# Kernel tuning notes

Hardware: AMD Instinct MI355X
Metric: run time of the kernel (lower is better)

The kernel has to match this reference:

```python
import jax, jax.numpy as jnp
import numpy as np

N, L, D = 1024, 128, 512
H = D // 2  # LSTM hidden per direction


def _lstm_dir(x, w_ih, w_hh, b_ih, b_hh, reverse=False):
    # x: [B, T, Din] -> [B, T, H]; PyTorch gate order i, f, g, o
    B = x.shape[0]
    Hh = w_hh.shape[1]
    xs = jnp.swapaxes(x, 0, 1)  # [T, B, Din]
    if reverse:
        xs = xs[::-1]
    pre = jnp.einsum('tbi,gi->tbg', xs, w_ih) + b_ih  # precompute input contribution

    def step(carry, p):
        h, c = carry
        g = p + h @ w_hh.T + b_hh
        i, f, cc, o = jnp.split(g, 4, axis=-1)
        c = jax.nn.sigmoid(f) * c + jax.nn.sigmoid(i) * jnp.tanh(cc)
        h = jax.nn.sigmoid(o) * jnp.tanh(c)
        return (h, c), h

    zeros = jnp.zeros((B, Hh), x.dtype)
    _, hs = jax.lax.scan(step, (zeros, zeros), pre)
    if reverse:
        hs = hs[::-1]
    return jnp.swapaxes(hs, 0, 1)


def _bilstm(x, params):
    # params: [(w_ih, w_hh, b_ih, b_hh)] for l0_fwd, l0_bwd, l1_fwd, l1_bwd
    for lf, lb in ((params[0], params[1]), (params[2], params[3])):
        f = _lstm_dir(x, *lf)
        b = _lstm_dir(x, *lb, reverse=True)
        x = jnp.concatenate([f, b], axis=-1)
    return x


def _forward(episodes, query, current_state, ages, Wq, bq, Wk, bk, lstm_params, k):
    # retrieve_relevant_episodes: batched version of the per-episode loop
    query_proj = query @ Wq.T + bq              # [D]
    emb = episodes.mean(axis=1)                 # [N, D] per-episode mean embedding
    key_proj = emb @ Wk.T + bk                  # [N, D]
    scores = key_proj @ query_proj              # [N] (matmul(q, kp.T).mean() == dot for 1D)
    _, idx = jax.lax.top_k(scores, k)           # descending, == argsort[-k:][::-1]
    sel = jnp.take(episodes, idx, axis=0)       # [k, L, D]
    # temporal_attention
    w = 1.0 / (1.0 + jnp.take(ages, idx) * 0.01)  # temporal recency weight
    x = sel * w[:, None, None]
    lstm_out = _bilstm(x, lstm_params)          # [k, L, D]
    att = jnp.einsum('d,kld->kl', current_state, lstm_out)  # [k, L] (== [k,1,L])
    attw = jax.nn.softmax(att, axis=-1)
    context = jnp.einsum('kl,kld->kd', attw, lstm_out)[:, None, :]  # [k, 1, D]
    return context


def setup_inputs() -> dict:
    key = jax.random.key(0)
    ks = jax.random.split(key, 32)
    s = 1.0 / np.sqrt(D)
    sh = 1.0 / np.sqrt(H)
    inp = {
        'episodes': jax.random.normal(ks[0], (N, L, D), jnp.float32),
        'query': jax.random.normal(ks[1], (D,), jnp.float32),
        'current_state': jax.random.normal(ks[2], (D,), jnp.float32),
        'ages': jax.random.uniform(ks[3], (N,), jnp.float32) * 100.0,
        'Wq': jax.random.normal(ks[4], (D, D), jnp.float32) * s,
        'bq': jnp.zeros((D,), jnp.float32),
        'Wk': jax.random.normal(ks[5], (D, D), jnp.float32) * s,
        'bk': jnp.zeros((D,), jnp.float32),
    }
    i = 6
    for name in ['l0', 'l0r', 'l1', 'l1r']:
        inp['w_ih_' + name] = jax.random.normal(ks[i], (4 * H, D), jnp.float32) * sh; i += 1
        inp['w_hh_' + name] = jax.random.normal(ks[i], (4 * H, H), jnp.float32) * sh; i += 1
        inp['b_ih_' + name] = jnp.zeros((4 * H,), jnp.float32)
        inp['b_hh_' + name] = jnp.zeros((4 * H,), jnp.float32)
    inp['k'] = 5
    return inp


def reference(episodes, query, current_state, ages, Wq, bq, Wk, bk,
              w_ih_l0, w_hh_l0, b_ih_l0, b_hh_l0,
              w_ih_l0r, w_hh_l0r, b_ih_l0r, b_hh_l0r,
              w_ih_l1, w_hh_l1, b_ih_l1, b_hh_l1,
              w_ih_l1r, w_hh_l1r, b_ih_l1r, b_hh_l1r, k):
    lstm_params = [
        (w_ih_l0, w_hh_l0, b_ih_l0, b_hh_l0),
        (w_ih_l0r, w_hh_l0r, b_ih_l0r, b_hh_l0r),
        (w_ih_l1, w_hh_l1, b_ih_l1, b_hh_l1),
        (w_ih_l1r, w_hh_l1r, b_ih_l1r, b_hh_l1r),
    ]
    return _forward(episodes, query, current_state, ages, Wq, bq, Wk, bk, lstm_params, k)
```

## Files before the change

### kernel.cpp

```cpp
#include <hip/hip_runtime.h>
#include <hip/hip_bf16.h>
#include <math.h>

typedef unsigned short u16;
typedef unsigned int   u32;
typedef unsigned long long u64;

#define DEV static __device__ __forceinline__

static constexpr int LL = 128, DD = 512, HH = 256, KK = 5, NN = 1024;

static constexpr size_t OFF_QP   = 0;
static constexpr size_t OFF_U    = 4096;
static constexpr size_t OFF_CC   = 8192;
static constexpr size_t OFF_SC   = 12288;
static constexpr size_t OFF_WSC  = 16384;
static constexpr size_t OFF_IDX  = 16640;
static constexpr size_t OFF_HG   = 20480;
static constexpr size_t OFF_PRE  = 102400;
static constexpr size_t OFF_OUT0 = OFF_PRE  + (size_t)2*LL*5*1024*4;
static constexpr size_t OFF_OUT1 = OFF_OUT0 + (size_t)5*LL*DD*4;

DEV float sigf(float x){ return 1.0f/(1.0f + expf(-x)); }

__global__ void k_qproj(const float* __restrict__ Wq, const float* __restrict__ q,
                        const float* __restrict__ bq, float* __restrict__ qp) {
  __shared__ float qs[512];
  int tid = threadIdx.x;
  qs[tid] = q[tid]; qs[tid+256] = q[tid+256];
  __syncthreads();
  int row  = blockIdx.x*8 + (tid >> 5);
  int lane = tid & 31;
  const float* wr = Wq + (size_t)row*512 + lane*16;
  float acc = 0.f;
  #pragma unroll
  for (int j = 0; j < 16; j += 4) {
    float4 w = *(const float4*)(wr + j);
    acc += w.x*qs[lane*16+j] + w.y*qs[lane*16+j+1] + w.z*qs[lane*16+j+2] + w.w*qs[lane*16+j+3];
  }
  #pragma unroll
  for (int off = 16; off > 0; off >>= 1) acc += __shfl_down(acc, off, 32);
  if (lane == 0) qp[row] = acc + bq[row];
}

__global__ void k_keyvec(const float* __restrict__ Wk, const float* __restrict__ bk,
                         const float* __restrict__ qp, float* __restrict__ u,
                         float* __restrict__ cconst) {
  __shared__ float qs[512];
  __shared__ float red[16][17];
  __shared__ float r2[256];
  int tid = threadIdx.x;
  qs[tid] = qp[tid]; qs[tid+256] = qp[tid+256];
  __syncthreads();
  int cl = tid & 15;
  int jc = tid >> 4;
  int col = blockIdx.x*16 + cl;
  float acc = 0.f;
  for (int j = jc*32; j < jc*32 + 32; ++j) acc += Wk[(size_t)j*512 + col] * qs[j];
  red[cl][jc] = acc;
  __syncthreads();
  if (tid < 16) {
    float a = 0.f;
    #pragma unroll
    for (int m = 0; m < 16; ++m) a += red[tid][m];
    u[blockIdx.x*16 + tid] = a;
  }
  if (blockIdx.x == 0) {
    float b2 = bk[tid]*qs[tid] + bk[tid+256]*qs[tid+256];
    r2[tid] = b2;
    __syncthreads();
    for (int off = 128; off > 0; off >>= 1) { if (tid < off) r2[tid] += r2[tid+off]; __syncthreads(); }
    if (tid == 0) cconst[0] = r2[0];
  }
}

__global__ void k_scores(const float* __restrict__ ep, const float* __restrict__ u,
                         const float* __restrict__ cconst, float* __restrict__ scores) {
  __shared__ float red[256];
  int tid = threadIdx.x, n = blockIdx.x;
  int d0 = (tid * 4) & 511;
  float u0 = u[d0+0], u1 = u[d0+1], u2 = u[d0+2], u3 = u[d0+3];
  const float* base = ep + (size_t)n * (LL*DD);
  float acc = 0.f;
  for (int c = tid; c < (LL*DD)/4; c += 256) {
    float4 v = *(const float4*)(base + (size_t)c*4);
    acc += v.x*u0 + v.y*u1 + v.z*u2 + v.w*u3;
  }
  red[tid] = acc;
  __syncthreads();
  for (int off = 128; off > 0; off >>= 1) { if (tid < off) red[tid] += red[tid+off]; __syncthreads(); }
  if (tid == 0) scores[n] = red[0] * (1.0f/LL) + cconst[0];
}

__global__ void k_topk(const float* __restrict__ scores, const float* __restrict__ ages,
                       int* __restrict__ idx5, float* __restrict__ wsc) {
  __shared__ float s0[NN];
  __shared__ float sv[NN];
  __shared__ int   si[NN];
  __shared__ int   chosen[KK];
  int tid = threadIdx.x;
  s0[tid] = scores[tid];
  __syncthreads();
  for (int r = 0; r < KK; ++r) {
    float v = s0[tid];
    for (int m = 0; m < r; ++m) if (chosen[m] == tid) v = -3.4e38f;
    sv[tid] = v; si[tid] = tid;
    __syncthreads();
    for (int off = 512; off > 0; off >>= 1) {
      if (tid < off) {
        float a = sv[tid], b = sv[tid+off];
        int ia = si[tid], ib = si[tid+off];
        if (b > a || (b == a && ib < ia)) { sv[tid] = b; si[tid] = ib; }
      }
      __syncthreads();
    }
    if (tid == 0) {
      int w = si[0];
      chosen[r] = w;
      idx5[r] = w;
      wsc[r] = 1.0f / (1.0f + ages[w] * 0.01f);
    }
    __syncthreads();
  }
}

__global__ void k_pre(const float* __restrict__ ep, const float* __restrict__ x1,
                      const int* __restrict__ idx5, const float* __restrict__ wsc,
                      const float* __restrict__ wihF, const float* __restrict__ wihB,
                      const float* __restrict__ bihF, const float* __restrict__ bhhF,
                      const float* __restrict__ bihB, const float* __restrict__ bhhB,
                      float* __restrict__ pre) {
  int t = blockIdx.x, rb = blockIdx.y, dir = blockIdx.z;
  int tid = threadIdx.x;
  __shared__ __align__(16) float xs[5*512];
  __shared__ __align__(16) float wt[256*36];
  if (ep) {
    for (int f = tid; f < 5*512; f += 256) {
      int b = f >> 9, i = f & 511;
      xs[f] = ep[((size_t)idx5[b]*LL + t)*DD + i] * wsc[b];
    }
  } else {
    for (int f = tid; f < 5*512; f += 256) {
      int b = f >> 9, i = f & 511;
      xs[f] = x1[((size_t)b*LL + t)*DD + i];
    }
  }
  const float* wih = dir ? wihB : wihF;
  const float* bih = dir ? bihB : bihF;
  const float* bhh = dir ? bhhB : bhhF;
  int r0 = rb * 256;
  float acc[5] = {0,0,0,0,0};
  for (int it = 0; it < 16; ++it) {
    __syncthreads();
    for (int c = tid; c < 2048; c += 256) {
      int rr = c >> 3;
      int ii = (c & 7) * 4;
      *(float4*)&wt[rr*36 + ii] = *(const float4*)&wih[(size_t)(r0+rr)*512 + it*32 + ii];
    }
    __syncthreads();
    const float* wrow = &wt[(size_t)tid*36];
    const float* xb = &xs[it*32];
    for (int ii = 0; ii < 32; ii += 4) {
      float4 w = *(const float4*)(wrow + ii);
      #pragma unroll
      for (int b = 0; b < 5; ++b) {
        float4 xv = *(const float4*)&xb[b*512 + ii];
        acc[b] += w.x*xv.x + w.y*xv.y + w.z*xv.z + w.w*xv.w;
      }
    }
  }
  int grow = r0 + tid;
  float bias = bih[grow] + bhh[grow];
  size_t pbase = (((size_t)dir*LL + t)*5)*1024 + grow;
  #pragma unroll
  for (int b = 0; b < 5; ++b) pre[pbase + (size_t)b*1024] = acc[b] + bias;
}

__global__ __launch_bounds__(1024) void k_lstm(
    const float* __restrict__ whhF, const float* __restrict__ whhB,
    const float* __restrict__ pre, float* __restrict__ out,
    u64* __restrict__ hg) {
  int wg  = blockIdx.x;
  int dir = wg >> 3;
  int q   = wg & 7;
  int tid = threadIdx.x;
  int p   = tid & 127;
  int jq  = tid >> 7;
  int jb  = jq * 32;
  const float* whh = dir ? whhB : whhF;

  __shared__ __align__(16) float h_lds[5*256];
  __shared__ float part[128*5*9];
  __shared__ float c_s[5*32];
  __shared__ float pre_lds[2*5*128];

  int gr = (p >> 5) * 256 + q * 32 + (p & 31);
  float w[32];
  #pragma unroll
  for (int m4 = 0; m4 < 8; ++m4) {
    float4 a = *(const float4*)(whh + (size_t)gr*256 + jb + m4*4);
    w[m4*4+0] = a.x; w[m4*4+1] = a.y; w[m4*4+2] = a.z; w[m4*4+3] = a.w;
  }
  for (int f = tid; f < 1280; f += 1024) h_lds[f] = 0.f;
  if (tid < 160) c_s[tid] = 0.f;
  u64* hg_dir = hg + (size_t)dir * 2 * 1280;

  if (tid < 640) {
    int t0 = dir ? (LL-1) : 0;
    int b = tid >> 7, r = tid & 127;
    int grow = (r >> 5)*256 + q*32 + (r & 31);
    pre_lds[tid] = pre[(((size_t)dir*LL + t0)*5 + b)*1024 + grow];
  }
  __syncthreads();

  for (int s = 0; s < LL; ++s) {
    int par = s & 1;
    int t = dir ? (LL-1-s) : s;
    float acc[5];
    #pragma unroll
    for (int b = 0; b < 5; ++b) {
      const float4* h4 = (const float4*)&h_lds[b*256 + jb];
      float a = 0.f;
      #pragma unroll
      for (int m4 = 0; m4 < 8; ++m4) {
        float4 hv = h4[m4];
        a += w[m4*4+0]*hv.x + w[m4*4+1]*hv.y + w[m4*4+2]*hv.z + w[m4*4+3]*hv.w;
      }
      acc[b] = a;
    }
    #pragma unroll
    for (int b = 0; b < 5; ++b) part[(p*5 + b)*9 + jq] = acc[b];
    __syncthreads();
    if (tid < 160) {
      int b = tid >> 5, u = tid & 31;
      float g[4];
      #pragma unroll
      for (int gate = 0; gate < 4; ++gate) {
        int r = gate*32 + u;
        float sum = pre_lds[par*640 + b*128 + r];
        #pragma unroll
        for (int m = 0; m < 8; ++m) sum += part[(r*5 + b)*9 + m];
        g[gate] = sum;
      }
      float ig = sigf(g[0]), fg = sigf(g[1]), cc = tanhf(g[2]), og = sigf(g[3]);
      float cn = fg * c_s[b*32 + u] + ig * cc;
      float hv = og * tanhf(cn);
      u64* hwr = hg_dir + (size_t)((s + 1) & 1) * 1280;
      u64 pk = ((u64)(u32)(s + 1) << 32) | (u64)__float_as_uint(hv);
      __hip_atomic_store(&hwr[b*256 + q*32 + u], pk,
                         __ATOMIC_RELAXED, __HIP_MEMORY_SCOPE_AGENT);
      c_s[b*32 + u] = cn;
      out[((size_t)b*LL + t)*DD + dir*HH + q*32 + u] = hv;
      h_lds[b*256 + q*32 + u] = hv;
    }
    float pfv = 0.f; int pfok = 0;
    if (tid >= 256 && tid < 896 && s + 1 < LL) {
      int f = tid - 256;
      int b = f >> 7, r = f & 127;
      int tn = dir ? (LL-2-s) : (s+1);
      int grow = (r >> 5)*256 + q*32 + (r & 31);
      pfv = pre[(((size_t)dir*LL + tn)*5 + b)*1024 + grow];
      pfok = 1;
    }
    if (tid >= 160 && s + 1 < LL) {
      int sp = s + 1;
      const u64* hrd = hg_dir + (size_t)(sp & 1) * 1280;
      int f0 = tid - 160;
      int f1 = f0 + 864;
      bool has2 = (f1 < 1280);
      u64 v0 = __hip_atomic_load(&hrd[f0], __ATOMIC_RELAXED, __HIP_MEMORY_SCOPE_AGENT);
      u64 v1 = has2 ? __hip_atomic_load(&hrd[f1], __ATOMIC_RELAXED, __HIP_MEMORY_SCOPE_AGENT)
                    : 0ull;
      bool d0 = false, d1 = !has2;
      while (!(d0 && d1)) {
        if (!d0) {
          if ((u32)(v0 >> 32) == (u32)sp) { h_lds[f0] = __uint_as_float((u32)v0); d0 = true; }
          else v0 = __hip_atomic_load(&hrd[f0], __ATOMIC_RELAXED, __HIP_MEMORY_SCOPE_AGENT);
        }
        if (!d1) {
          if ((u32)(v1 >> 32) == (u32)sp) { h_lds[f1] = __uint_as_float((u32)v1); d1 = true; }
          else v1 = __hip_atomic_load(&hrd[f1], __ATOMIC_RELAXED, __HIP_MEMORY_SCOPE_AGENT);
        }
      }
    }
    if (pfok) pre_lds[((par^1))*640 + (tid - 256)] = pfv;
    __syncthreads();
  }
}

__global__ void k_attn(const float* __restrict__ out1, const float* __restrict__ csb,
                       float* __restrict__ outp) {
  int b = blockIdx.x, tid = threadIdx.x;
  __shared__ float cs[512];
  __shared__ float att[128];
  __shared__ float red[256];
  __shared__ float smax, ssum;
  cs[tid] = csb[tid]; cs[tid+256] = csb[tid+256];
  __syncthreads();
  {
    int t = tid & 127, half = tid >> 7;
    const float* row = out1 + ((size_t)b*LL + t)*DD + half*256;
    const float* c2 = cs + half*256;
    float a = 0.f;
    for (int d = 0; d < 256; ++d) a += row[d] * c2[d];
    red[tid] = a;
  }
  __syncthreads();
  if (tid < 128) att[tid] = red[tid] + red[tid+128];
  __syncthreads();
  if (tid < 64) red[tid] = fmaxf(att[tid], att[tid+64]);
  __syncthreads();
  if (tid == 0) { float m = red[0]; for (int o = 1; o < 64; ++o) m = fmaxf(m, red[o]); smax = m; }
  __syncthreads();
  if (tid < 128) att[tid] = expf(att[tid] - smax);
  __syncthreads();
  if (tid < 64) red[tid] = att[tid] + att[tid+64];
  __syncthreads();
  if (tid == 0) { float s = 0.f; for (int o = 0; o < 64; ++o) s += red[o]; ssum = s; }
  __syncthreads();
  float inv = 1.0f / ssum;
  for (int d = tid; d < DD; d += 256) {
    float acc = 0.f;
    for (int t2 = 0; t2 < LL; ++t2) acc += att[t2] * out1[((size_t)b*LL + t2)*DD + d];
    outp[b*DD + d] = acc * inv;
  }
}

extern "C" void kernel_launch(void* const* d_in, const int* in_sizes, int n_in,
                              void* d_out, int out_size, void* d_ws, size_t ws_size,
                              hipStream_t stream) {
  (void)in_sizes; (void)n_in; (void)out_size; (void)ws_size;
  const float* ep   = (const float*)d_in[0];
  const float* qu   = (const float*)d_in[1];
  const float* cst  = (const float*)d_in[2];
  const float* ages = (const float*)d_in[3];
  const float* Wq   = (const float*)d_in[4];
  const float* bq   = (const float*)d_in[5];
  const float* Wk   = (const float*)d_in[6];
  const float* bk   = (const float*)d_in[7];
  const float *wih[4], *whh[4], *bih[4], *bhh[4];
  for (int l = 0; l < 4; ++l) {
    wih[l] = (const float*)d_in[8 + l*4 + 0];
    whh[l] = (const float*)d_in[8 + l*4 + 1];
    bih[l] = (const float*)d_in[8 + l*4 + 2];
    bhh[l] = (const float*)d_in[8 + l*4 + 3];
  }
  char* ws = (char*)d_ws;
  float* qp   = (float*)(ws + OFF_QP);
  float* uvec = (float*)(ws + OFF_U);
  float* cc   = (float*)(ws + OFF_CC);
  float* sc   = (float*)(ws + OFF_SC);
  float* wsc  = (float*)(ws + OFF_WSC);
  int*   idx5 = (int*)  (ws + OFF_IDX);
  u64*   hg0  = (u64*)  (ws + OFF_HG);
  u64*   hg1  = (u64*)  (ws + OFF_HG + 40960);
  float* pre  = (float*)(ws + OFF_PRE);
  float* out0 = (float*)(ws + OFF_OUT0);
  float* out1 = (float*)(ws + OFF_OUT1);

  hipMemsetAsync(ws + OFF_HG, 0, 81920, stream);

  k_qproj <<<64, 256, 0, stream>>>(Wq, qu, bq, qp);
  k_keyvec<<<32, 256, 0, stream>>>(Wk, bk, qp, uvec, cc);
  k_scores<<<NN, 256, 0, stream>>>(ep, uvec, cc, sc);
  k_topk  <<<1, 1024, 0, stream>>>(sc, ages, idx5, wsc);

  k_pre <<<dim3(LL,4,2), 256, 0, stream>>>(ep, nullptr, idx5, wsc,
        wih[0], wih[1], bih[0], bhh[0], bih[1], bhh[1], pre);
  k_lstm<<<16, 1024, 0, stream>>>(whh[0], whh[1], pre, out0, hg0);

  k_pre <<<dim3(LL,4,2), 256, 0, stream>>>(nullptr, out0, idx5, wsc,
        wih[2], wih[3], bih[2], bhh[2], bih[3], bhh[3], pre);
  k_lstm<<<16, 1024, 0, stream>>>(whh[2], whh[3], pre, out1, hg1);

  k_attn<<<KK, 256, 0, stream>>>(out1, cst, (float*)d_out);
}
```

Measured before the change: 1.525 ms.

## Interleave forward and backward LSTM directions in one workgroup to hide exchange latency

Each workgroup now handles one hidden slice for both directions, holding both recurrent weight slices in registers and alternating forward and backward steps. While one direction's gate math runs, the other threads poll the global h exchange for the opposite direction, so cross-workgroup sync latency overlaps with compute. A lighter barrier macro replaces __syncthreads. The grid is halved to 8 workgroups, which doubles register pressure per thread and puts both directions' serial work on the same workgroups.

```diff
diff --git a/kernel.cpp b/kernel.cpp
--- a/kernel.cpp
+++ b/kernel.cpp
@@ -22,6 +22,12 @@
 static constexpr size_t OFF_OUT1 = OFF_OUT0 + (size_t)5*LL*DD*4;
 
 DEV float sigf(float x){ return 1.0f/(1.0f + expf(-x)); }
+
+#define WGBAR() do { \
+  asm volatile("s_waitcnt lgkmcnt(0)" ::: "memory"); \
+  __builtin_amdgcn_s_barrier(); \
+  __builtin_amdgcn_sched_barrier(0); \
+} while (0)
 
 __global__ void k_qproj(const float* __restrict__ Wq, const float* __restrict__ q,
                         const float* __restrict__ bq, float* __restrict__ qp) {
@@ -180,111 +186,186 @@
     const float* __restrict__ whhF, const float* __restrict__ whhB,
     const float* __restrict__ pre, float* __restrict__ out,
     u64* __restrict__ hg) {
-  int wg  = blockIdx.x;
-  int dir = wg >> 3;
-  int q   = wg & 7;
+  int q   = blockIdx.x;
   int tid = threadIdx.x;
   int p   = tid & 127;
   int jq  = tid >> 7;
   int jb  = jq * 32;
-  const float* whh = dir ? whhB : whhF;
-
-  __shared__ __align__(16) float h_lds[5*256];
+
+  __shared__ __align__(16) float hF[5*256];
+  __shared__ __align__(16) float hB[5*256];
   __shared__ float part[128*5*9];
-  __shared__ float c_s[5*32];
-  __shared__ float pre_lds[2*5*128];
+  __shared__ float csF[160], csB[160];
+  __shared__ float preF[2*640], preB[2*640];
 
   int gr = (p >> 5) * 256 + q * 32 + (p & 31);
-  float w[32];
+  float wf[32], wb[32];
   #pragma unroll
   for (int m4 = 0; m4 < 8; ++m4) {
-    float4 a = *(const float4*)(whh + (size_t)gr*256 + jb + m4*4);
-    w[m4*4+0] = a.x; w[m4*4+1] = a.y; w[m4*4+2] = a.z; w[m4*4+3] = a.w;
-  }
-  for (int f = tid; f < 1280; f += 1024) h_lds[f] = 0.f;
-  if (tid < 160) c_s[tid] = 0.f;
-  u64* hg_dir = hg + (size_t)dir * 2 * 1280;
+    float4 a = *(const float4*)(whhF + (size_t)gr*256 + jb + m4*4);
+    wf[m4*4+0] = a.x; wf[m4*4+1] = a.y; wf[m4*4+2] = a.z; wf[m4*4+3] = a.w;
+    float4 c = *(const float4*)(whhB + (size_t)gr*256 + jb + m4*4);
+    wb[m4*4+0] = c.x; wb[m4*4+1] = c.y; wb[m4*4+2] = c.z; wb[m4*4+3] = c.w;
+  }
+  for (int f = tid; f < 1280; f += 1024) { hF[f] = 0.f; hB[f] = 0.f; }
+  if (tid < 160) { csF[tid] = 0.f; csB[tid] = 0.f; }
+  u64* hgF = hg;
+  u64* hgB = hg + 2560;
 
   if (tid < 640) {
-    int t0 = dir ? (LL-1) : 0;
     int b = tid >> 7, r = tid & 127;
     int grow = (r >> 5)*256 + q*32 + (r & 31);
-    pre_lds[tid] = pre[(((size_t)dir*LL + t0)*5 + b)*1024 + grow];
+    preF[tid] = pre[((size_t)(0*LL + 0)*5 + b)*1024 + grow];
+    preB[tid] = pre[((size_t)(1*LL + (LL-1))*5 + b)*1024 + grow];
   }
   __syncthreads();
 
   for (int s = 0; s < LL; ++s) {
-    int par = s & 1;
-    int t = dir ? (LL-1-s) : s;
-    float acc[5];
-    #pragma unroll
-    for (int b = 0; b < 5; ++b) {
-      const float4* h4 = (const float4*)&h_lds[b*256 + jb];
-      float a = 0.f;
-      #pragma unroll
-      for (int m4 = 0; m4 < 8; ++m4) {
-        float4 hv = h4[m4];
-        a += w[m4*4+0]*hv.x + w[m4*4+1]*hv.y + w[m4*4+2]*hv.z + w[m4*4+3]*hv.w;
-      }
-      acc[b] = a;
-    }
-    #pragma unroll
-    for (int b = 0; b < 5; ++b) part[(p*5 + b)*9 + jq] = acc[b];
-    __syncthreads();
+    int par  = s & 1;
+    int parn = (s + 1) & 1;
+    int tF = s, tB = LL - 1 - s;
+
+    {
+      float acc[5];
+      #pragma unroll
+      for (int b = 0; b < 5; ++b) {
+        const float4* h4 = (const float4*)&hF[b*256 + jb];
+        float a = 0.f;
+        #pragma unroll
+        for (int m4 = 0; m4 < 8; ++m4) {
+          float4 hv = h4[m4];
+          a += wf[m4*4+0]*hv.x + wf[m4*4+1]*hv.y + wf[m4*4+2]*hv.z + wf[m4*4+3]*hv.w;
+        }
+        acc[b] = a;
+      }
+      #pragma unroll
+      for (int b = 0; b < 5; ++b) part[(p*5 + b)*9 + jq] = acc[b];
+    }
+    WGBAR();
+
     if (tid < 160) {
       int b = tid >> 5, u = tid & 31;
       float g[4];
       #pragma unroll
       for (int gate = 0; gate < 4; ++gate) {
         int r = gate*32 + u;
-        float sum = pre_lds[par*640 + b*128 + r];
+        float sum = preF[par*640 + b*128 + r];
         #pragma unroll
         for (int m = 0; m < 8; ++m) sum += part[(r*5 + b)*9 + m];
         g[gate] = sum;
       }
       float ig = sigf(g[0]), fg = sigf(g[1]), cc = tanhf(g[2]), og = sigf(g[3]);
-      float cn = fg * c_s[b*32 + u] + ig * cc;
+      float cn = fg * csF[tid] + ig * cc;
       float hv = og * tanhf(cn);
-      u64* hwr = hg_dir + (size_t)((s + 1) & 1) * 1280;
       u64 pk = ((u64)(u32)(s + 1) << 32) | (u64)__float_as_uint(hv);
-      __hip_atomic_store(&hwr[b*256 + q*32 + u], pk,
+      __hip_atomic_store(&hgF[parn*1280 + b*256 + q*32 + u], pk,
                          __ATOMIC_RELAXED, __HIP_MEMORY_SCOPE_AGENT);
-      c_s[b*32 + u] = cn;
-      out[((size_t)b*LL + t)*DD + dir*HH + q*32 + u] = hv;
-      h_lds[b*256 + q*32 + u] = hv;
-    }
-    float pfv = 0.f; int pfok = 0;
-    if (tid >= 256 && tid < 896 && s + 1 < LL) {
-      int f = tid - 256;
-      int b = f >> 7, r = f & 127;
-      int tn = dir ? (LL-2-s) : (s+1);
-      int grow = (r >> 5)*256 + q*32 + (r & 31);
-      pfv = pre[(((size_t)dir*LL + tn)*5 + b)*1024 + grow];
-      pfok = 1;
-    }
-    if (tid >= 160 && s + 1 < LL) {
-      int sp = s + 1;
-      const u64* hrd = hg_dir + (size_t)(sp & 1) * 1280;
-      int f0 = tid - 160;
-      int f1 = f0 + 864;
-      bool has2 = (f1 < 1280);
-      u64 v0 = __hip_atomic_load(&hrd[f0], __ATOMIC_RELAXED, __HIP_MEMORY_SCOPE_AGENT);
-      u64 v1 = has2 ? __hip_atomic_load(&hrd[f1], __ATOMIC_RELAXED, __HIP_MEMORY_SCOPE_AGENT)
-                    : 0ull;
-      bool d0 = false, d1 = !has2;
-      while (!(d0 && d1)) {
-        if (!d0) {
-          if ((u32)(v0 >> 32) == (u32)sp) { h_lds[f0] = __uint_as_float((u32)v0); d0 = true; }
-          else v0 = __hip_atomic_load(&hrd[f0], __ATOMIC_RELAXED, __HIP_MEMORY_SCOPE_AGENT);
+      csF[tid] = cn;
+      out[((size_t)b*LL + tF)*DD + 0*HH + q*32 + u] = hv;
+      hF[b*256 + q*32 + u] = hv;
+    } else {
+      float pfv = 0.f; int pfok = 0;
+      if (tid < 800 && s + 1 < LL) {
+        int f = tid - 160;
+        int b = f >> 7, r = f & 127;
+        int grow = (r >> 5)*256 + q*32 + (r & 31);
+        pfv = pre[((size_t)(1*LL + (tB - 1))*5 + b)*1024 + grow];
+        pfok = 1;
+      }
+      if (s > 0) {
+        const u64* hrd = hgB + (size_t)par * 1280;
+        u32 sp = (u32)s;
+        int f0 = tid - 160;
+        int f1 = f0 + 864;
+        bool has2 = (f1 < 1280);
+        u64 v0 = __hip_atomic_load(&hrd[f0], __ATOMIC_RELAXED, __HIP_MEMORY_SCOPE_AGENT);
+        u64 v1 = has2 ? __hip_atomic_load(&hrd[f1], __ATOMIC_RELAXED, __HIP_MEMORY_SCOPE_AGENT) : 0ull;
+        bool d0 = false, d1 = !has2;
+        while (!(d0 && d1)) {
+          if (!d0) {
+            if ((u32)(v0 >> 32) == sp) { hB[f0] = __uint_as_float((u32)v0); d0 = true; }
+            else v0 = __hip_atomic_load(&hrd[f0], __ATOMIC_RELAXED, __HIP_MEMORY_SCOPE_AGENT);
+          }
+          if (!d1) {
+            if ((u32)(v1 >> 32) == sp) { hB[f1] = __uint_as_float((u32)v1); d1 = true; }
+            else v1 = __hip_atomic_load(&hrd[f1], __ATOMIC_RELAXED, __HIP_MEMORY_SCOPE_AGENT);
+          }
         }
-        if (!d1) {
-          if ((u32)(v1 >> 32) == (u32)sp) { h_lds[f1] = __uint_as_float((u32)v1); d1 = true; }
-          else v1 = __hip_atomic_load(&hrd[f1], __ATOMIC_RELAXED, __HIP_MEMORY_SCOPE_AGENT);
+      }
+      if (pfok) preB[parn*640 + (tid - 160)] = pfv;
+    }
+    WGBAR();
+
+    {
+      float acc[5];
+      #pragma unroll
+      for (int b = 0; b < 5; ++b) {
+        const float4* h4 = (const float4*)&hB[b*256 + jb];
+        float a = 0.f;
+        #pragma unroll
+        for (int m4 = 0; m4 < 8; ++m4) {
+          float4 hv = h4[m4];
+          a += wb[m4*4+0]*hv.x + wb[m4*4+1]*hv.y + wb[m4*4+2]*hv.z + wb[m4*4+3]*hv.w;
         }
-      }
-    }
-    if (pfok) pre_lds[((par^1))*640 + (tid - 256)] = pfv;
-    __syncthreads();
+        acc[b] = a;
+      }
+      #pragma unroll
+      for (int b = 0; b < 5; ++b) part[(p*5 + b)*9 + jq] = acc[b];
+    }
+    WGBAR();
+
+    if (tid < 160) {
+      int b = tid >> 5, u = tid & 31;
+      float g[4];
+      #pragma unroll
+      for (int gate = 0; gate < 4; ++gate) {
+        int r = gate*32 + u;
+        float sum = preB[par*640 + b*128 + r];
+        #pragma unroll
+        for (int m = 0; m < 8; ++m) sum += part[(r*5 + b)*9 + m];
+        g[gate] = sum;
+      }
+      float ig = sigf(g[0]), fg = sigf(g[1]), cc = tanhf(g[2]), og = sigf(g[3]);
+      float cn = fg * csB[tid] + ig * cc;
+      float hv = og * tanhf(cn);
+      u64 pk = ((u64)(u32)(s + 1) << 32) | (u64)__float_as_uint(hv);
+      __hip_atomic_store(&hgB[parn*1280 + b*256 + q*32 + u], pk,
+                         __ATOMIC_RELAXED, __HIP_MEMORY_SCOPE_AGENT);
+      csB[tid] = cn;
+      out[((size_t)b*LL + tB)*DD + 1*HH + q*32 + u] = hv;
+      hB[b*256 + q*32 + u] = hv;
+    } else {
+      float pfv = 0.f; int pfok = 0;
+      if (tid < 800 && s + 1 < LL) {
+        int f = tid - 160;
+        int b = f >> 7, r = f & 127;
+        int grow = (r >> 5)*256 + q*32 + (r & 31);
+        pfv = pre[((size_t)(0*LL + (tF + 1))*5 + b)*1024 + grow];
+        pfok = 1;
+      }
+      if (s + 1 < LL) {
+        const u64* hrd = hgF + (size_t)parn * 1280;
+        u32 sp = (u32)(s + 1);
+        int f0 = tid - 160;
+        int f1 = f0 + 864;
+        bool has2 = (f1 < 1280);
+        u64 v0 = __hip_atomic_load(&hrd[f0], __ATOMIC_RELAXED, __HIP_MEMORY_SCOPE_AGENT);
+        u64 v1 = has2 ? __hip_atomic_load(&hrd[f1], __ATOMIC_RELAXED, __HIP_MEMORY_SCOPE_AGENT) : 0ull;
+        bool d0 = false, d1 = !has2;
+        while (!(d0 && d1)) {
+          if (!d0) {
+            if ((u32)(v0 >> 32) == sp) { hF[f0] = __uint_as_float((u32)v0); d0 = true; }
+            else v0 = __hip_atomic_load(&hrd[f0], __ATOMIC_RELAXED, __HIP_MEMORY_SCOPE_AGENT);
+          }
+          if (!d1) {
+            if ((u32)(v1 >> 32) == sp) { hF[f1] = __uint_as_float((u32)v1); d1 = true; }
+            else v1 = __hip_atomic_load(&hrd[f1], __ATOMIC_RELAXED, __HIP_MEMORY_SCOPE_AGENT);
+          }
+        }
+      }
+      if (pfok) preF[parn*640 + (tid - 160)] = pfv;
+    }
+    WGBAR();
   }
 }
 
@@ -367,11 +448,11 @@
 
   k_pre <<<dim3(LL,4,2), 256, 0, stream>>>(ep, nullptr, idx5, wsc,
         wih[0], wih[1], bih[0], bhh[0], bih[1], bhh[1], pre);
-  k_lstm<<<16, 1024, 0, stream>>>(whh[0], whh[1], pre, out0, hg0);
+  k_lstm<<<8, 1024, 0, stream>>>(whh[0], whh[1], pre, out0, hg0);
 
   k_pre <<<dim3(LL,4,2), 256, 0, stream>>>(nullptr, out0, idx5, wsc,
         wih[2], wih[3], bih[2], bhh[2], bih[3], bhh[3], pre);
-  k_lstm<<<16, 1024, 0, stream>>>(whh[2], whh[3], pre, out1, hg1);
+  k_lstm<<<8, 1024, 0, stream>>>(whh[2], whh[3], pre, out1, hg1);
 
   k_attn<<<KK, 256, 0, stream>>>(out1, cst, (float*)d_out);
 }
```

New measurement: 2.054 ms. 34.7% more time.
